# Kernel tuning notes

Hardware: AMD Instinct MI355X
Metric: run time of the kernel (lower is better)

## Reference

```python
import jax, jax.numpy as jnp
import numpy as np

B, H, T, D, R = 2, 12, 2048, 64, 16
D_STD = D - R


def setup_inputs() -> dict:
    key = jax.random.key(0)
    ks = jax.random.split(key, 5)
    return {
        "Q": jax.random.normal(ks[0], (B, H, T, D), jnp.float32),
        "K": jax.random.normal(ks[1], (B, H, T, D), jnp.float32),
        "V": jax.random.normal(ks[2], (B, H, T, D), jnp.float32),
        "d_bias": jax.random.normal(ks[3], (B, H, T), jnp.float32),
        "W_recip": jax.random.normal(ks[4], (D, R), jnp.float32) * 0.02,
        "w_std": jnp.full((H,), 0.5, jnp.float32),
        "w_rec": jnp.full((H,), 0.3, jnp.float32),
        "w_disc": jnp.full((H,), 0.2, jnp.float32),
    }


def reference(Q, K, V, d_bias, W_recip, w_std, w_rec, w_disc):
    b, h, t, d = Q.shape
    r = W_recip.shape[1]
    d_std = d - r
    sq_std = jnp.sqrt(w_std)[None, :, None, None]  # [1,H,1,1]
    sq_rec = jnp.sqrt(w_rec)[None, :, None, None]
    Q_low = jnp.einsum("bhtd,dr->bhtr", Q, W_recip)  # [B,H,T,R]
    K_low = jnp.einsum("bhtd,dr->bhtr", K, W_recip)
    Q_aug = jnp.concatenate([sq_std * Q[..., :d_std], sq_rec * K_low], axis=-1)  # [B,H,T,D]
    K_aug = jnp.concatenate([sq_std * K[..., :d_std], sq_rec * Q_low], axis=-1)
    scale = 1.0 / jnp.sqrt(jnp.asarray(d, Q.dtype))
    scores = jnp.einsum("bhqd,bhkd->bhqk", Q_aug, K_aug) * scale  # [B,H,T,T]
    # rank-1 additive bias, broadcast over queries: bias[b,h,q,k] = w_disc[h]*d_bias[b,h,k]
    scores = scores + (w_disc[None, :, None, None] * d_bias[:, :, None, :])
    causal = jnp.tril(jnp.ones((t, t), bool))  # [T,T]
    scores = jnp.where(causal[None, None], scores, -jnp.inf)
    attn = jax.nn.softmax(scores, axis=-1)
    return jnp.einsum("bhqk,bhkd->bhqd", attn, V)
```

## Files before the change

kernel.cpp:

```cpp
#include <hip/hip_runtime.h>
#include <math.h>

#define T_SEQ 2048
#define NH    12
#define NB    2
#define BHC   (NB*NH)
#define NQT   32

typedef _Float16 half4_t __attribute__((ext_vector_type(4)));
typedef _Float16 half8_t __attribute__((ext_vector_type(8)));
typedef float    floatx4 __attribute__((ext_vector_type(4)));

__device__ __forceinline__ half8_t h8splat(_Float16 s) {
  return (half8_t){s, s, s, s, s, s, s, s};
}

__global__ __launch_bounds__(256) void prep_kernel(
    const float* __restrict__ Q, const float* __restrict__ K,
    const float* __restrict__ V, const float* __restrict__ W,
    const float* __restrict__ wstd, const float* __restrict__ wrec,
    const float* __restrict__ dbias, const float* __restrict__ wdisc,
    ushort* __restrict__ QF, ushort* __restrict__ KF, ushort* __restrict__ VF,
    float* __restrict__ B2)
{
  __shared__ __align__(16) _Float16 Qsh[64*72];
  __shared__ __align__(16) _Float16 Ksh[64*72];
  __shared__ __align__(16) _Float16 Vsh[64*72];
  __shared__ __align__(16) _Float16 Lqh[64*16];
  __shared__ __align__(16) _Float16 Lkh[64*16];

  const int tid = threadIdx.x;
  const int w = tid >> 6, lane = tid & 63;
  const int quad = lane >> 4, ln = lane & 15;
  const int bh = blockIdx.x >> 5, tblk = blockIdx.x & 31;
  const long g0 = ((long)bh * T_SEQ + tblk * 64) * 64;

  const float4* gQ = (const float4*)(Q + g0);
  const float4* gK = (const float4*)(K + g0);
  const float4* gV = (const float4*)(V + g0);
  for (int i = tid; i < 1024; i += 256) {
    int r = i >> 4, c4 = i & 15;
    float4 q = gQ[i], k = gK[i], v = gV[i];
    *(half4_t*)&Qsh[r*72 + c4*4] = (half4_t){(_Float16)q.x,(_Float16)q.y,(_Float16)q.z,(_Float16)q.w};
    *(half4_t*)&Ksh[r*72 + c4*4] = (half4_t){(_Float16)k.x,(_Float16)k.y,(_Float16)k.z,(_Float16)k.w};
    *(half4_t*)&Vsh[r*72 + c4*4] = (half4_t){(_Float16)v.x,(_Float16)v.y,(_Float16)v.z,(_Float16)v.w};
  }
  __syncthreads();

  half4_t bw[4];
#pragma unroll
  for (int dk = 0; dk < 4; dk++)
#pragma unroll
    for (int i = 0; i < 4; i++)
      bw[dk][i] = (_Float16)W[(dk*16 + quad*4 + i)*16 + ln];

  floatx4 cq = {0.f,0.f,0.f,0.f}, ck = {0.f,0.f,0.f,0.f};
#pragma unroll
  for (int dk = 0; dk < 4; dk++) {
    half4_t aq = *(const half4_t*)&Qsh[(w*16 + ln)*72 + dk*16 + quad*4];
    half4_t ak = *(const half4_t*)&Ksh[(w*16 + ln)*72 + dk*16 + quad*4];
    cq = __builtin_amdgcn_mfma_f32_16x16x16f16(aq, bw[dk], cq, 0, 0, 0);
    ck = __builtin_amdgcn_mfma_f32_16x16x16f16(ak, bw[dk], ck, 0, 0, 0);
  }
#pragma unroll
  for (int i = 0; i < 4; i++) {
    Lqh[(w*16 + quad*4 + i)*16 + ln] = (_Float16)cq[i];
    Lkh[(w*16 + quad*4 + i)*16 + ln] = (_Float16)ck[i];
  }
  __syncthreads();

  const int h = bh % NH;
  const float sstd = sqrtf(wstd[h]);
  const float srec = sqrtf(wrec[h]);
  const half8_t hq_std = h8splat((_Float16)(0.125f * sstd));
  const half8_t hk_std = h8splat((_Float16)sstd);
  const half8_t hq_rec = h8splat((_Float16)(0.125f * srec));
  const half8_t hk_rec = h8splat((_Float16)srec);

  if (tid < 64) B2[(long)bh*T_SEQ + tblk*64 + tid] =
      wdisc[h] * dbias[(long)bh*T_SEQ + tblk*64 + tid];

#pragma unroll
  for (int cc = 0; cc < 2; cc++) {
    int c = tid + cc * 256;
    {
      int lp = c & 63, dp = (c >> 6) & 1, rt = c >> 7;
      int row = rt*16 + (lp & 15);
      int d0 = dp*32 + (lp >> 4)*8;
      half8_t hq, hk;
      if (d0 < 48) {
        hq = *(const half8_t*)&Qsh[row*72 + d0] * hq_std;
        hk = *(const half8_t*)&Ksh[row*72 + d0] * hk_std;
      } else {
        hq = *(const half8_t*)&Lkh[row*16 + (d0-48)] * hq_rec;
        hk = *(const half8_t*)&Lqh[row*16 + (d0-48)] * hk_rec;
      }
      long tile16 = (long)bh*128 + tblk*4 + rt;
      ((int4*)QF)[tile16*128 + dp*64 + lp] = *(int4*)&hq;
      ((int4*)KF)[tile16*128 + dp*64 + lp] = *(int4*)&hk;
    }
    {
      int lv = c & 63, nt = (c >> 6) & 3, v2 = c >> 8;
      int d = nt*16 + (lv & 15), qv = lv >> 4;
      half8_t hv;
#pragma unroll
      for (int j = 0; j < 4; j++) {
        hv[j]   = Vsh[(v2*32 + qv*4 + j)*72 + d];
        hv[4+j] = Vsh[(v2*32 + 16 + qv*4 + j)*72 + d];
      }
      ((int4*)VF)[((long)bh*32 + tblk)*512 + (v2*4 + nt)*64 + lv] = *(int4*)&hv;
    }
  }
}

__global__ __launch_bounds__(64, 3) void flash_kernel(
    const ushort* __restrict__ QF, const ushort* __restrict__ KF,
    const ushort* __restrict__ VF, const float* __restrict__ B2,
    float* __restrict__ Out)
{
  const int lane = threadIdx.x;
  const int quad = lane >> 4, ln = lane & 15;
  const int bid = blockIdx.x;
  const int bh  = bid % BHC;
  const int t16 = 127 - bid / BHC;
  const int qrow = t16*16 + ln;
  const int ktmax = t16 >> 2;

  const ushort* gK = KF + (long)bh * 131072;
  const ushort* gV = VF + (long)bh * 131072;
  const float*  gB = B2 + (long)bh * T_SEQ;

  half8_t bq[2];
  {
    const ushort* gQ = QF + ((long)bh*128 + t16) * 1024;
    bq[0] = *(const half8_t*)(gQ + lane*8);
    bq[1] = *(const half8_t*)(gQ + 512 + lane*8);
  }

  float m_i = -1e30f, l_i = 0.f;
  floatx4 acc[4];
#pragma unroll
  for (int nt = 0; nt < 4; nt++) acc[nt] = (floatx4){0.f,0.f,0.f,0.f};

  half8_t kf[8], vf[8];
#pragma unroll
  for (int c = 0; c < 8; c++) {
    kf[c] = *(const half8_t*)(gK + c*512 + lane*8);
    vf[c] = *(const half8_t*)(gV + c*512 + lane*8);
  }

  for (int kt = 0; kt <= ktmax; kt++) {
    const long onx = (long)(kt < ktmax ? kt + 1 : kt) * 4096;

    floatx4 st[4];
#pragma unroll
    for (int mt = 0; mt < 4; mt++) {
      floatx4 c = (floatx4){0.f,0.f,0.f,0.f};
      c = __builtin_amdgcn_mfma_f32_16x16x32_f16(kf[mt*2],     bq[0], c, 0, 0, 0);
      c = __builtin_amdgcn_mfma_f32_16x16x32_f16(kf[mt*2 + 1], bq[1], c, 0, 0, 0);
      st[mt] = c;
    }
#pragma unroll
    for (int c = 0; c < 8; c++)
      kf[c] = *(const half8_t*)(gK + onx + c*512 + lane*8);

    const bool diag = (kt == ktmax);
    float rowmax = -1e30f;
#pragma unroll
    for (int mt = 0; mt < 4; mt++) {
      float4 bb = *(const float4*)(gB + kt*64 + mt*16 + quad*4);
      float bv[4] = {bb.x, bb.y, bb.z, bb.w};
#pragma unroll
      for (int i = 0; i < 4; i++) {
        float v = st[mt][i] + bv[i];
        int key = kt*64 + mt*16 + quad*4 + i;
        if (diag && key > qrow) v = -1e30f;
        st[mt][i] = v;
        rowmax = fmaxf(rowmax, v);
      }
    }
    rowmax = fmaxf(rowmax, __shfl_xor(rowmax, 16));
    rowmax = fmaxf(rowmax, __shfl_xor(rowmax, 32));
    float mnew  = fmaxf(m_i, rowmax);
    float alpha = __expf(m_i - mnew);
    float psum = 0.f;
    half4_t pa[4];
#pragma unroll
    for (int mt = 0; mt < 4; mt++)
#pragma unroll
      for (int i = 0; i < 4; i++) {
        float p = __expf(st[mt][i] - mnew);
        psum += p;
        pa[mt][i] = (_Float16)p;
      }
    psum += __shfl_xor(psum, 16);
    psum += __shfl_xor(psum, 32);
    l_i = l_i * alpha + psum;
    m_i = mnew;

    float af[4];
#pragma unroll
    for (int i = 0; i < 4; i++) af[i] = __shfl(alpha, quad*4 + i);
#pragma unroll
    for (int nt = 0; nt < 4; nt++)
#pragma unroll
      for (int i = 0; i < 4; i++) acc[nt][i] *= af[i];

#pragma unroll
    for (int v2 = 0; v2 < 2; v2++)
#pragma unroll
      for (int nt = 0; nt < 4; nt++) {
        half8_t vv = vf[v2*4 + nt];
        half4_t b0 = __builtin_shufflevector(vv, vv, 0,1,2,3);
        half4_t b1 = __builtin_shufflevector(vv, vv, 4,5,6,7);
        acc[nt] = __builtin_amdgcn_mfma_f32_16x16x16f16(pa[2*v2],   b0, acc[nt], 0, 0, 0);
        acc[nt] = __builtin_amdgcn_mfma_f32_16x16x16f16(pa[2*v2+1], b1, acc[nt], 0, 0, 0);
      }
#pragma unroll
    for (int c = 0; c < 8; c++)
      vf[c] = *(const half8_t*)(gV + onx + c*512 + lane*8);
  }

  float lr[4];
#pragma unroll
  for (int i = 0; i < 4; i++) lr[i] = 1.f / __shfl(l_i, quad*4 + i);
  const long obase = (long)bh*T_SEQ*64 + (long)(t16*16)*64;
#pragma unroll
  for (int i = 0; i < 4; i++)
#pragma unroll
    for (int nt = 0; nt < 4; nt++)
      Out[obase + (quad*4 + i)*64 + nt*16 + ln] = acc[nt][i] * lr[i];
}

extern "C" void kernel_launch(void* const* d_in, const int* in_sizes, int n_in,
                              void* d_out, int out_size, void* d_ws, size_t ws_size,
                              hipStream_t stream) {
  const float* Q     = (const float*)d_in[0];
  const float* K     = (const float*)d_in[1];
  const float* V     = (const float*)d_in[2];
  const float* dbias = (const float*)d_in[3];
  const float* W     = (const float*)d_in[4];
  const float* wstd  = (const float*)d_in[5];
  const float* wrec  = (const float*)d_in[6];
  const float* wdisc = (const float*)d_in[7];
  float* Out = (float*)d_out;

  const long NEL = (long)BHC * T_SEQ * 64;
  ushort* QF = (ushort*)d_ws;
  ushort* KF = QF + NEL;
  ushort* VF = KF + NEL;
  float*  B2 = (float*)(VF + NEL);

  prep_kernel<<<BHC * NQT, 256, 0, stream>>>(Q, K, V, W, wstd, wrec, dbias, wdisc,
                                             QF, KF, VF, B2);
  flash_kernel<<<BHC * 128, 64, 0, stream>>>(QF, KF, VF, B2, Out);
}
```

Baseline: 133.0 us.

## Group four query tiles per 256-thread block and peel the diagonal key tile

The flash kernel now launches 256-thread blocks in which four waves handle four adjacent 16-row query tiles that share the same key-tile range, so K/V loads can hit cache together. The causal diagonal tile is peeled out of the main loop, which removes the per-element mask check from the steady-state iterations. The bias is preloaded and fed into the MFMA accumulator init, so the separate add is dropped. Each wave still loads K/V into registers on its own rather than through shared memory, so reuse relies on L1/L2 hits, and the coarser blocks give fewer, larger work units, which may affect load balance across CUs.

```diff
diff --git a/kernel.cpp b/kernel.cpp
--- a/kernel.cpp
+++ b/kernel.cpp
@@ -113,18 +113,19 @@
   }
 }
 
-__global__ __launch_bounds__(64, 3) void flash_kernel(
+__global__ __launch_bounds__(256, 3) void flash_kernel(
     const ushort* __restrict__ QF, const ushort* __restrict__ KF,
     const ushort* __restrict__ VF, const float* __restrict__ B2,
     float* __restrict__ Out)
 {
-  const int lane = threadIdx.x;
+  const int tid = threadIdx.x;
+  const int w = tid >> 6, lane = tid & 63;
   const int quad = lane >> 4, ln = lane & 15;
   const int bid = blockIdx.x;
   const int bh  = bid % BHC;
-  const int t16 = 127 - bid / BHC;
+  const int g   = 31 - bid / BHC;
+  const int t16 = 4*g + w;
   const int qrow = t16*16 + ln;
-  const int ktmax = t16 >> 2;
 
   const ushort* gK = KF + (long)bh * 131072;
   const ushort* gV = VF + (long)bh * 131072;
@@ -143,19 +144,23 @@
   for (int nt = 0; nt < 4; nt++) acc[nt] = (floatx4){0.f,0.f,0.f,0.f};
 
   half8_t kf[8], vf[8];
+  float4 bbc[4];
 #pragma unroll
   for (int c = 0; c < 8; c++) {
     kf[c] = *(const half8_t*)(gK + c*512 + lane*8);
     vf[c] = *(const half8_t*)(gV + c*512 + lane*8);
   }
-
-  for (int kt = 0; kt <= ktmax; kt++) {
-    const long onx = (long)(kt < ktmax ? kt + 1 : kt) * 4096;
+#pragma unroll
+  for (int mt = 0; mt < 4; mt++)
+    bbc[mt] = *(const float4*)(gB + mt*16 + quad*4);
+
+  for (int kt = 0; kt < g; kt++) {
+    const long onx = (long)(kt + 1) * 4096;
 
     floatx4 st[4];
 #pragma unroll
     for (int mt = 0; mt < 4; mt++) {
-      floatx4 c = (floatx4){0.f,0.f,0.f,0.f};
+      floatx4 c = (floatx4){bbc[mt].x, bbc[mt].y, bbc[mt].z, bbc[mt].w};
       c = __builtin_amdgcn_mfma_f32_16x16x32_f16(kf[mt*2],     bq[0], c, 0, 0, 0);
       c = __builtin_amdgcn_mfma_f32_16x16x32_f16(kf[mt*2 + 1], bq[1], c, 0, 0, 0);
       st[mt] = c;
@@ -163,22 +168,15 @@
 #pragma unroll
     for (int c = 0; c < 8; c++)
       kf[c] = *(const half8_t*)(gK + onx + c*512 + lane*8);
-
-    const bool diag = (kt == ktmax);
+#pragma unroll
+    for (int mt = 0; mt < 4; mt++)
+      bbc[mt] = *(const float4*)(gB + (kt+1)*64 + mt*16 + quad*4);
+
     float rowmax = -1e30f;
 #pragma unroll
-    for (int mt = 0; mt < 4; mt++) {
-      float4 bb = *(const float4*)(gB + kt*64 + mt*16 + quad*4);
-      float bv[4] = {bb.x, bb.y, bb.z, bb.w};
-#pragma unroll
-      for (int i = 0; i < 4; i++) {
-        float v = st[mt][i] + bv[i];
-        int key = kt*64 + mt*16 + quad*4 + i;
-        if (diag && key > qrow) v = -1e30f;
-        st[mt][i] = v;
-        rowmax = fmaxf(rowmax, v);
-      }
-    }
+    for (int mt = 0; mt < 4; mt++)
+#pragma unroll
+      for (int i = 0; i < 4; i++) rowmax = fmaxf(rowmax, st[mt][i]);
     rowmax = fmaxf(rowmax, __shfl_xor(rowmax, 16));
     rowmax = fmaxf(rowmax, __shfl_xor(rowmax, 32));
     float mnew  = fmaxf(m_i, rowmax);
@@ -219,6 +217,64 @@
 #pragma unroll
     for (int c = 0; c < 8; c++)
       vf[c] = *(const half8_t*)(gV + onx + c*512 + lane*8);
+  }
+
+  {
+    floatx4 st[4];
+#pragma unroll
+    for (int mt = 0; mt < 4; mt++) {
+      floatx4 c = (floatx4){bbc[mt].x, bbc[mt].y, bbc[mt].z, bbc[mt].w};
+      c = __builtin_amdgcn_mfma_f32_16x16x32_f16(kf[mt*2],     bq[0], c, 0, 0, 0);
+      c = __builtin_amdgcn_mfma_f32_16x16x32_f16(kf[mt*2 + 1], bq[1], c, 0, 0, 0);
+      st[mt] = c;
+    }
+    float rowmax = -1e30f;
+#pragma unroll
+    for (int mt = 0; mt < 4; mt++)
+#pragma unroll
+      for (int i = 0; i < 4; i++) {
+        int key = g*64 + mt*16 + quad*4 + i;
+        float v = (key > qrow) ? -1e30f : st[mt][i];
+        st[mt][i] = v;
+        rowmax = fmaxf(rowmax, v);
+      }
+    rowmax = fmaxf(rowmax, __shfl_xor(rowmax, 16));
+    rowmax = fmaxf(rowmax, __shfl_xor(rowmax, 32));
+    float mnew  = fmaxf(m_i, rowmax);
+    float alpha = __expf(m_i - mnew);
+    float psum = 0.f;
+    half4_t pa[4];
+#pragma unroll
+    for (int mt = 0; mt < 4; mt++)
+#pragma unroll
+      for (int i = 0; i < 4; i++) {
+        float p = __expf(st[mt][i] - mnew);
+        psum += p;
+        pa[mt][i] = (_Float16)p;
+      }
+    psum += __shfl_xor(psum, 16);
+    psum += __shfl_xor(psum, 32);
+    l_i = l_i * alpha + psum;
+    m_i = mnew;
+
+    float af[4];
+#pragma unroll
+    for (int i = 0; i < 4; i++) af[i] = __shfl(alpha, quad*4 + i);
+#pragma unroll
+    for (int nt = 0; nt < 4; nt++)
+#pragma unroll
+      for (int i = 0; i < 4; i++) acc[nt][i] *= af[i];
+
+#pragma unroll
+    for (int v2 = 0; v2 < 2; v2++)
+#pragma unroll
+      for (int nt = 0; nt < 4; nt++) {
+        half8_t vv = vf[v2*4 + nt];
+        half4_t b0 = __builtin_shufflevector(vv, vv, 0,1,2,3);
+        half4_t b1 = __builtin_shufflevector(vv, vv, 4,5,6,7);
+        acc[nt] = __builtin_amdgcn_mfma_f32_16x16x16f16(pa[2*v2],   b0, acc[nt], 0, 0, 0);
+        acc[nt] = __builtin_amdgcn_mfma_f32_16x16x16f16(pa[2*v2+1], b1, acc[nt], 0, 0, 0);
+      }
   }
 
   float lr[4];
@@ -253,5 +309,5 @@
 
   prep_kernel<<<BHC * NQT, 256, 0, stream>>>(Q, K, V, W, wstd, wrec, dbias, wdisc,
                                              QF, KF, VF, B2);
-  flash_kernel<<<BHC * 128, 64, 0, stream>>>(QF, KF, VF, B2, Out);
+  flash_kernel<<<BHC * NQT, 256, 0, stream>>>(QF, KF, VF, B2, Out);
 }
```

New measurement: 133.8 us. No clear change (+0.6%).
